# Performance work log

Measured on AMD Instinct MI355X. Metric: run time of the kernel, lower is better.

The kernel has to match this reference:

```python
import jax, jax.numpy as jnp
import numpy as np

HIDDEN = 4096
N_HEADS = 32
HEAD_DIM = HIDDEN // N_HEADS  # 128
ROPE_BASE = 10000.0


def _rotate_half(x):
    h = x.shape[-1] // 2
    return jnp.concatenate((-x[..., h:], x[..., :h]), axis=-1)


def _rope_sin_cos(position_ids):
    # position_ids: [B, S] int -> sin, cos: [B, 1, S, head_dim]
    inv_freq = 1.0 / (ROPE_BASE ** (jnp.arange(0, HEAD_DIM, 2, dtype=jnp.float32) / HEAD_DIM))
    freqs = position_ids.astype(jnp.float32)[..., None] * inv_freq  # [B,S,hd/2]
    emb = jnp.concatenate((freqs, freqs), axis=-1)  # [B,S,hd]
    return jnp.sin(emb)[:, None, :, :], jnp.cos(emb)[:, None, :, :]


def setup_inputs() -> dict:
    key = jax.random.key(0)
    k1, k2, k3 = jax.random.split(key, 3)
    B, S = 2, 2048
    hidden_states = jax.random.normal(k1, (B, S, HIDDEN), dtype=jnp.float32)
    w_qkv = jax.random.normal(k2, (HIDDEN, 3 * HIDDEN), dtype=jnp.float32) * 0.02
    wo = jax.random.normal(k3, (HIDDEN, HIDDEN), dtype=jnp.float32) * 0.02
    position_ids = jnp.broadcast_to(jnp.arange(S, dtype=jnp.int32)[None, :], (B, S))
    return {"hidden_states": hidden_states, "w_qkv": w_qkv, "wo": wo,
            "position_ids": position_ids}


def reference(hidden_states, w_qkv, wo, position_ids):
    B, S, H = hidden_states.shape
    qkv = hidden_states @ w_qkv  # [B,S,3H]
    q, k, v = jnp.split(qkv, 3, axis=-1)
    # [B,S,nH,hd] -> [B,nH,S,hd]
    q = q.reshape(B, S, N_HEADS, HEAD_DIM).transpose(0, 2, 1, 3)
    k = k.reshape(B, S, N_HEADS, HEAD_DIM).transpose(0, 2, 1, 3)
    v = v.reshape(B, S, N_HEADS, HEAD_DIM).transpose(0, 2, 1, 3)
    sin, cos = _rope_sin_cos(position_ids)  # [B,1,S,hd]
    q = q * cos + _rotate_half(q) * sin
    k = k * cos + _rotate_half(k) * sin
    scale = 1.0 / np.sqrt(HEAD_DIM)
    scores = jnp.einsum('bhqd,bhkd->bhqk', q, k) * scale
    causal = jnp.tril(jnp.ones((S, S), dtype=bool))
    scores = jnp.where(causal[None, None, :, :], scores, jnp.finfo(scores.dtype).min)
    attn = jax.nn.softmax(scores, axis=-1)
    out = jnp.einsum('bhqk,bhkd->bhqd', attn, v)  # [B,nH,S,hd]
    out = out.transpose(0, 2, 1, 3).reshape(B, S, H)
    return out @ wo
```

## Files before the change

### kernel.cpp

```cpp
#include <hip/hip_runtime.h>

typedef unsigned int u32;
typedef unsigned short u16;
typedef short short8 __attribute__((ext_vector_type(8)));
typedef float f32x4 __attribute__((ext_vector_type(4)));
typedef unsigned short us4 __attribute__((ext_vector_type(4)));

#define S_LEN 2048
#define BATCH 2
#define HID 4096
#define NH 32
#define HD 128
#define TRIH 12288

#define GCAST(p) ((const __attribute__((address_space(1))) u32*)(p))
#define LCAST(p) ((__attribute__((address_space(3))) u32*)(p))

static __device__ __forceinline__ u16 f2bf(float f) {
  union { float f; u32 u; } x; x.f = f;
  u32 u = x.u;
  u32 r = u + 0x7FFFu + ((u >> 16) & 1u);
  return (u16)(r >> 16);
}
static __device__ __forceinline__ float bf2f(u16 h) {
  union { u32 u; float f; } x; x.u = ((u32)h) << 16;
  return x.f;
}

__global__ __launch_bounds__(256) void cvt_f32_bf16(const float* __restrict__ in,
                                                    u16* __restrict__ out, int n4) {
  int i = blockIdx.x * 256 + threadIdx.x;
  if (i >= n4) return;
  float4 v = ((const float4*)in)[i];
  us4 o;
  o.x = f2bf(v.x); o.y = f2bf(v.y); o.z = f2bf(v.z); o.w = f2bf(v.w);
  ((us4*)out)[i] = o;
}

__global__ __launch_bounds__(256) void tr_cvt(const float* __restrict__ in,
                                              u16* __restrict__ out, int R, int C) {
  __shared__ float tile[32][33];
  int c0 = blockIdx.x * 32, r0 = blockIdx.y * 32;
  int tx = threadIdx.x, ty = threadIdx.y;
  for (int i = ty; i < 32; i += 8)
    tile[i][tx] = in[(size_t)(r0 + i) * C + c0 + tx];
  __syncthreads();
  for (int i = ty; i < 32; i += 8)
    out[(size_t)(c0 + i) * R + r0 + tx] = f2bf(tile[tx][i]);
}


template<int MQ, int NQ>
static __device__ __forceinline__ void mfma_quad(f32x4 (&acc)[8][4], short8 (&af)[4][2],
                                                 short8 (&bfr)[4][2]) {
#pragma unroll
  for (int ml = 0; ml < 4; ++ml)
#pragma unroll
    for (int nl = 0; nl < 2; ++nl) {
      acc[MQ*4+ml][NQ*2+nl] = __builtin_amdgcn_mfma_f32_16x16x32_bf16(
          af[ml][0], bfr[NQ*2+nl][0], acc[MQ*4+ml][NQ*2+nl], 0, 0, 0);
      acc[MQ*4+ml][NQ*2+nl] = __builtin_amdgcn_mfma_f32_16x16x32_bf16(
          af[ml][1], bfr[NQ*2+nl][1], acc[MQ*4+ml][NQ*2+nl], 0, 0, 0);
    }
}

template<int MQ>
static __device__ __forceinline__ void read_a(short8 (&af)[4][2], const u16* abase, int lane) {
#pragma unroll
  for (int ml = 0; ml < 4; ++ml) {
    int r = MQ*64 + ml*16 + (lane & 15);
#pragma unroll
    for (int kh = 0; kh < 2; ++kh) {
      int j = kh*4 + (lane >> 4);
      af[ml][kh] = *(const short8*)(abase + r*64 + ((j ^ (r & 7)) << 3));
    }
  }
}
template<int NQ>
static __device__ __forceinline__ void read_b(short8 (&bfr)[4][2], const u16* bbase,
                                              int rbase, int lane) {
#pragma unroll
  for (int nl = 0; nl < 2; ++nl) {
    int r = rbase + (NQ*2+nl)*16 + (lane & 15);
#pragma unroll
    for (int kh = 0; kh < 2; ++kh) {
      int j = kh*4 + (lane >> 4);
      bfr[NQ*2+nl][kh] = *(const short8*)(bbase + r*64 + ((j ^ (r & 7)) << 3));
    }
  }
}

#define PHASE_CLOSE() \
  __builtin_amdgcn_s_barrier(); \
  __builtin_amdgcn_sched_barrier(0);

#define SEAM_CLOSE(NSTR) \
  asm volatile("s_waitcnt vmcnt(" NSTR ")" ::: "memory"); \
  __builtin_amdgcn_s_barrier(); \
  __builtin_amdgcn_sched_barrier(0);

template<int OUTF32>
__global__ __launch_bounds__(512, 1) void gemm256(const u16* __restrict__ A,
                                                  const u16* __restrict__ Bt,
                                                  void* __restrict__ Cout,
                                                  int M, int N, int K, int nbm) {
  __shared__ __attribute__((aligned(16))) u16 lds[65536];
  const int tid = threadIdx.x, wave = tid >> 6, lane = tid & 63;
  const int wr = wave >> 2, wc = wave & 3;
  const int nwg = gridDim.x, wg = blockIdx.x, cpx = nwg >> 3;
  const int swz = (wg & 7) * cpx + (wg >> 3);
  const size_t tileM = (size_t)(swz % nbm) * 256;
  const size_t tileN = (size_t)(swz / nbm) * 256;
  const int nIter = K >> 7;

  const int r_ = tid >> 3;
  const int gc_ = (tid & 7) ^ (r_ & 7);

  const u16* Ag = A + tileM * K;
  const u16* Bg = Bt + tileN * K;

  f32x4 acc[8][4] = {};
  short8 af[4][2], bfr[4][2];

  auto stageA = [&](int kt, int buf, int half) {
    const u16* g0 = Ag + (size_t)(half*128 + r_) * K + kt*64 + (gc_ << 3);
    u16* l = lds + buf*16384 + half*8192 + wave*512;
    __builtin_amdgcn_global_load_lds(GCAST(g0), LCAST(l), 16, 0, 0);
    __builtin_amdgcn_global_load_lds(GCAST(g0 + (size_t)64*K), LCAST(l + 4096), 16, 0, 0);
  };
  auto stageB = [&](int kt, int buf, int half) {
    const u16* g0 = Bg + (size_t)(half*128 + r_) * K + kt*64 + (gc_ << 3);
    u16* l = lds + 32768 + buf*16384 + half*8192 + wave*512;
    __builtin_amdgcn_global_load_lds(GCAST(g0), LCAST(l), 16, 0, 0);
    __builtin_amdgcn_global_load_lds(GCAST(g0 + (size_t)64*K), LCAST(l + 4096), 16, 0, 0);
  };

  const u16* a0 = lds + wr*8192;
  const u16* a1 = lds + 16384 + wr*8192;
  const u16* b0 = lds + 32768 + (wc >> 1)*8192;
  const u16* b1 = lds + 32768 + 16384 + (wc >> 1)*8192;
  const int brb = (wc & 1) * 64;

  stageA(0, 0, 0); stageA(0, 0, 1);
  stageB(0, 0, 0); stageB(0, 0, 1);
  stageB(1, 1, 0); stageB(1, 1, 1);
  SEAM_CLOSE("4")

  for (int i = 0; i < nIter; ++i) {
    const int t1 = 2*i + 1, t2 = 2*i + 2, t3 = 2*i + 3;
    const bool more = (i + 1 < nIter);

    read_a<0>(af, a0, lane);
    read_b<0>(bfr, b0, brb, lane);
    read_b<1>(bfr, b0, brb, lane);
    stageA(t1, 1, 0); stageA(t1, 1, 1);
    __builtin_amdgcn_s_setprio(1);
    mfma_quad<0, 0>(acc, af, bfr);
    mfma_quad<0, 1>(acc, af, bfr);
    __builtin_amdgcn_s_setprio(0);
    PHASE_CLOSE()

    read_a<1>(af, a0, lane);
    if (more) { stageB(t2, 0, 0); stageB(t2, 0, 1); }
    __builtin_amdgcn_s_setprio(1);
    mfma_quad<1, 0>(acc, af, bfr);
    mfma_quad<1, 1>(acc, af, bfr);
    __builtin_amdgcn_s_setprio(0);
    if (more) { SEAM_CLOSE("4") } else { SEAM_CLOSE("0") }

    read_a<0>(af, a1, lane);
    read_b<0>(bfr, b1, brb, lane);
    read_b<1>(bfr, b1, brb, lane);
    if (more) { stageA(t2, 0, 0); stageA(t2, 0, 1); }
    __builtin_amdgcn_s_setprio(1);
    mfma_quad<0, 0>(acc, af, bfr);
    mfma_quad<0, 1>(acc, af, bfr);
    __builtin_amdgcn_s_setprio(0);
    PHASE_CLOSE()

    read_a<1>(af, a1, lane);
    if (more) { stageB(t3, 1, 0); stageB(t3, 1, 1); }
    __builtin_amdgcn_s_setprio(1);
    mfma_quad<1, 0>(acc, af, bfr);
    mfma_quad<1, 1>(acc, af, bfr);
    __builtin_amdgcn_s_setprio(0);
    if (more) { SEAM_CLOSE("4") } else { PHASE_CLOSE() }
  }

  const int r0o = (lane >> 4) << 2, c0o = lane & 15;
#pragma unroll
  for (int m = 0; m < 8; ++m)
#pragma unroll
    for (int n = 0; n < 4; ++n)
#pragma unroll
      for (int rr = 0; rr < 4; ++rr) {
        size_t grow = tileM + wr*128 + m*16 + r0o + rr;
        size_t gcol = tileN + wc*64 + n*16 + c0o;
        if (OUTF32) ((float*)Cout)[grow * N + gcol] = acc[m][n][rr];
        else        ((u16*)Cout)[grow * N + gcol] = f2bf(acc[m][n][rr]);
      }
}

__global__ __launch_bounds__(256) void rope_kernel(u16* __restrict__ qkv,
                                                   const int* __restrict__ pid) {
  int idx = blockIdx.x * 256 + threadIdx.x;
  int row = idx >> 12;
  int rem = idx & 4095;
  int which = rem >> 11;
  int rem2 = rem & 2047;
  int h = rem2 >> 6;
  int j = rem2 & 63;
  u16* p = qkv + (size_t)row * TRIH + which * HID + h * HD + j;
  float x0 = bf2f(p[0]), x1 = bf2f(p[64]);
  float pos = (float)pid[row];
  float invf = expf(-(float)j * 0.14391156831212787f);
  float th = pos * invf;
  float sn, cs;
  sincosf(th, &sn, &cs);
  p[0]  = f2bf(x0 * cs - x1 * sn);
  p[64] = f2bf(x1 * cs + x0 * sn);
}

__global__ __launch_bounds__(512, 2) void attn_kernel(const u16* __restrict__ qkv,
                                                      u16* __restrict__ O) {
  const int bid = blockIdx.x;
  const int qt = 15 - (bid >> 6);
  const int bh = bid & 63;
  const int b = bh >> 5, h = bh & 31;
  const int tid = threadIdx.x, wave = tid >> 6, lane = tid & 63;
  __shared__ u16 Ks[64 * 128];
  __shared__ u16 VsT[128 * 64];
  __shared__ u16 Ps[8][16 * 64];
  const u16* base = qkv + (size_t)b * S_LEN * TRIH + h * HD;

  const int rbase = (lane >> 4) << 2;
  const int cbase = lane & 15;
  const int q_lo = qt * 128;
  const int wrow0 = q_lo + wave * 16;

  short8 qf[4];
  {
    const u16* qrow = base + (size_t)(wrow0 + cbase) * TRIH;
#pragma unroll
    for (int f = 0; f < 4; ++f)
      qf[f] = *(const short8*)(qrow + ((f * 4 + (lane >> 4)) << 3));
  }

  const int tmax_w = 2 * qt + (wave >= 4 ? 1 : 0);
  const int tmax_b = 2 * qt + 1;

  float mrun[4], lrun[4];
  f32x4 accO[8] = {};
#pragma unroll
  for (int r = 0; r < 4; ++r) { mrun[r] = -1e30f; lrun[r] = 0.f; }

  short8 kreg[2], vreg[2];
#pragma unroll
  for (int it = 0; it < 2; ++it) {
    int c = tid + it * 512;
    int row = c >> 4, ch = c & 15;
    const u16* src = base + (size_t)row * TRIH + (ch << 3);
    kreg[it] = *(const short8*)(src + HID);
    vreg[it] = *(const short8*)(src + 2 * HID);
  }

  for (int t = 0; t <= tmax_b; ++t) {
    __syncthreads();
#pragma unroll
    for (int it = 0; it < 2; ++it) {
      int c = tid + it * 512;
      int row = c >> 4, ch = c & 15;
      *(short8*)(Ks + row * 128 + ((ch ^ (row & 7)) << 3)) = kreg[it];
#pragma unroll
      for (int i = 0; i < 8; ++i) {
        int d = (ch << 3) + i;
        VsT[d * 64 + (((row >> 3) ^ (ch & 7)) << 3) + (row & 7)] = (u16)vreg[it][i];
      }
    }
    __syncthreads();

    if (t < tmax_b) {
      int kv1 = (t + 1) << 6;
#pragma unroll
      for (int it = 0; it < 2; ++it) {
        int c = tid + it * 512;
        int row = c >> 4, ch = c & 15;
        const u16* src = base + (size_t)(kv1 + row) * TRIH + (ch << 3);
        kreg[it] = *(const short8*)(src + HID);
        vreg[it] = *(const short8*)(src + 2 * HID);
      }
    }

    if (t > tmax_w) continue;

    f32x4 s[4] = {};
#pragma unroll
    for (int n = 0; n < 4; ++n) {
      int krow = n * 16 + cbase;
#pragma unroll
      for (int f = 0; f < 4; ++f) {
        int ch = f * 4 + (lane >> 4);
        short8 kf = *(const short8*)(Ks + krow * 128 + ((ch ^ (krow & 7)) << 3));
        s[n] = __builtin_amdgcn_mfma_f32_16x16x32_bf16(qf[f], kf, s[n], 0, 0, 0);
      }
    }
    const float scale = 0.08838834764831845f;
    const int kv0 = t << 6;
    if (t == tmax_w) {
#pragma unroll
      for (int n = 0; n < 4; ++n)
#pragma unroll
        for (int r = 0; r < 4; ++r) {
          int kvcol = kv0 + n * 16 + cbase;
          int qrow = wrow0 + rbase + r;
          s[n][r] = (kvcol <= qrow) ? s[n][r] * scale : -1e30f;
        }
    } else {
#pragma unroll
      for (int n = 0; n < 4; ++n) s[n] *= scale;
    }

    float tmax[4];
#pragma unroll
    for (int r = 0; r < 4; ++r) {
      float tm = fmaxf(fmaxf(s[0][r], s[1][r]), fmaxf(s[2][r], s[3][r]));
      tm = fmaxf(tm, __shfl_xor(tm, 1));
      tm = fmaxf(tm, __shfl_xor(tm, 2));
      tm = fmaxf(tm, __shfl_xor(tm, 4));
      tm = fmaxf(tm, __shfl_xor(tm, 8));
      tmax[r] = tm;
    }
    bool need = false;
#pragma unroll
    for (int r = 0; r < 4; ++r) need |= (tmax[r] > mrun[r] + 8.0f);
    if (__any(need)) {
#pragma unroll
      for (int r = 0; r < 4; ++r) {
        float mnew = fmaxf(mrun[r], tmax[r]);
        float corr = __expf(mrun[r] - mnew);
        float rs = 0.f;
#pragma unroll
        for (int n = 0; n < 4; ++n) { float pv = __expf(s[n][r] - mnew); s[n][r] = pv; rs += pv; }
        rs += __shfl_xor(rs, 1); rs += __shfl_xor(rs, 2);
        rs += __shfl_xor(rs, 4); rs += __shfl_xor(rs, 8);
        lrun[r] = lrun[r] * corr + rs;
        mrun[r] = mnew;
#pragma unroll
        for (int nd = 0; nd < 8; ++nd) accO[nd][r] *= corr;
      }
    } else {
#pragma unroll
      for (int r = 0; r < 4; ++r) {
        float rs = 0.f;
#pragma unroll
        for (int n = 0; n < 4; ++n) { float pv = __expf(s[n][r] - mrun[r]); s[n][r] = pv; rs += pv; }
        rs += __shfl_xor(rs, 1); rs += __shfl_xor(rs, 2);
        rs += __shfl_xor(rs, 4); rs += __shfl_xor(rs, 8);
        lrun[r] += rs;
      }
    }

    u16* Pw = (u16*)Ps[wave];
#pragma unroll
    for (int n = 0; n < 4; ++n)
#pragma unroll
      for (int r = 0; r < 4; ++r) {
        int rl = rbase + r;
        int col = n * 16 + cbase;
        Pw[rl * 64 + (((col >> 3) ^ (rl & 7)) << 3) + (col & 7)] = f2bf(s[n][r]);
      }

    short8 pa[2];
    {
      int prow = lane & 15;
#pragma unroll
      for (int f2 = 0; f2 < 2; ++f2) {
        int ch = f2 * 4 + (lane >> 4);
        pa[f2] = *(const short8*)(Pw + prow * 64 + ((ch ^ (prow & 7)) << 3));
      }
    }
#pragma unroll
    for (int nd = 0; nd < 8; ++nd) {
      int drow = nd * 16 + cbase;
#pragma unroll
      for (int f2 = 0; f2 < 2; ++f2) {
        int ch = f2 * 4 + (lane >> 4);
        short8 vb = *(const short8*)(VsT + drow * 64 + ((ch ^ ((drow >> 3) & 7)) << 3));
        accO[nd] = __builtin_amdgcn_mfma_f32_16x16x32_bf16(pa[f2], vb, accO[nd], 0, 0, 0);
      }
    }
  }

#pragma unroll
  for (int nd = 0; nd < 8; ++nd)
#pragma unroll
    for (int r = 0; r < 4; ++r) {
      int qrow = wrow0 + rbase + r;
      int col = h * HD + nd * 16 + cbase;
      O[(size_t)(b * S_LEN + qrow) * HID + col] = f2bf(accO[nd][r] / lrun[r]);
    }
}

extern "C" void kernel_launch(void* const* d_in, const int* in_sizes, int n_in,
                              void* d_out, int out_size, void* d_ws, size_t ws_size,
                              hipStream_t stream) {
  const float* hidden = (const float*)d_in[0];
  const float* w_qkv  = (const float*)d_in[1];
  const float* wo     = (const float*)d_in[2];
  const int*   pid    = (const int*)d_in[3];

  const size_t MB = 1024ull * 1024ull;
  u16* hb    = (u16*)d_ws;
  u16* wqkvT = (u16*)((char*)d_ws + 32 * MB);
  u16* woT   = (u16*)((char*)d_ws + 128 * MB);
  u16* qkvb  = (u16*)((char*)d_ws + 160 * MB);
  u16* Obuf  = hb;

  cvt_f32_bf16<<<16384, 256, 0, stream>>>(hidden, hb, (BATCH * S_LEN * HID) / 4);
  dim3 tb(32, 8);
  tr_cvt<<<dim3(TRIH / 32, HID / 32), tb, 0, stream>>>(w_qkv, wqkvT, HID, TRIH);
  tr_cvt<<<dim3(HID / 32, HID / 32), tb, 0, stream>>>(wo, woT, HID, HID);

  gemm256<0><<<768, 512, 0, stream>>>(hb, wqkvT, qkvb, BATCH * S_LEN, TRIH, HID, 16);

  rope_kernel<<<(BATCH * S_LEN * 2 * NH * 64) / 256, 256, 0, stream>>>(qkvb, pid);

  attn_kernel<<<1024, 512, 0, stream>>>(qkvb, Obuf);

  gemm256<1><<<256, 512, 0, stream>>>(Obuf, woT, d_out, BATCH * S_LEN, HID, HID, 16);
}
```

Measured before the change: 822.0 us.

## Double-buffer K/V tiles in attention and vectorize RoPE kernel

The attention kernel now keeps two shared-memory K/V buffers and writes the next tile into the alternate buffer while the current one is computed. This drops one __syncthreads per iteration and lets global loads run two tiles ahead. Shared memory per block grows from about 48KB to about 80KB, which may limit blocks per CU. Separately, the RoPE kernel now has each thread handle 8 contiguous elements with 16-byte vector loads and stores instead of scalar u16 accesses, with the grid shrunk to match.

```diff
diff --git a/kernel.cpp b/kernel.cpp
--- a/kernel.cpp
+++ b/kernel.cpp
@@ -204,21 +204,27 @@
 __global__ __launch_bounds__(256) void rope_kernel(u16* __restrict__ qkv,
                                                    const int* __restrict__ pid) {
   int idx = blockIdx.x * 256 + threadIdx.x;
-  int row = idx >> 12;
-  int rem = idx & 4095;
-  int which = rem >> 11;
-  int rem2 = rem & 2047;
-  int h = rem2 >> 6;
-  int j = rem2 & 63;
-  u16* p = qkv + (size_t)row * TRIH + which * HID + h * HD + j;
-  float x0 = bf2f(p[0]), x1 = bf2f(p[64]);
+  int row = idx >> 9;
+  int rem = idx & 511;
+  int which = rem >> 8;
+  int h = (rem >> 3) & 31;
+  int j0 = (rem & 7) << 3;
+  u16* p = qkv + (size_t)row * TRIH + which * HID + h * HD + j0;
+  short8 lo = *(short8*)p;
+  short8 hi = *(short8*)(p + 64);
   float pos = (float)pid[row];
-  float invf = expf(-(float)j * 0.14391156831212787f);
-  float th = pos * invf;
-  float sn, cs;
-  sincosf(th, &sn, &cs);
-  p[0]  = f2bf(x0 * cs - x1 * sn);
-  p[64] = f2bf(x1 * cs + x0 * sn);
+  short8 olo, ohi;
+#pragma unroll
+  for (int i = 0; i < 8; ++i) {
+    float x0 = bf2f((u16)lo[i]), x1 = bf2f((u16)hi[i]);
+    float th = pos * expf(-(float)(j0 + i) * 0.14391156831212787f);
+    float sn, cs;
+    sincosf(th, &sn, &cs);
+    olo[i] = (short)f2bf(x0 * cs - x1 * sn);
+    ohi[i] = (short)f2bf(x1 * cs + x0 * sn);
+  }
+  *(short8*)p = olo;
+  *(short8*)(p + 64) = ohi;
 }
 
 __global__ __launch_bounds__(512, 2) void attn_kernel(const u16* __restrict__ qkv,
@@ -228,8 +234,8 @@
   const int bh = bid & 63;
   const int b = bh >> 5, h = bh & 31;
   const int tid = threadIdx.x, wave = tid >> 6, lane = tid & 63;
-  __shared__ u16 Ks[64 * 128];
-  __shared__ u16 VsT[128 * 64];
+  __shared__ u16 Ks[2][64 * 128];
+  __shared__ u16 VsT[2][128 * 64];
   __shared__ u16 Ps[8][16 * 64];
   const u16* base = qkv + (size_t)b * S_LEN * TRIH + h * HD;
 
@@ -255,41 +261,40 @@
   for (int r = 0; r < 4; ++r) { mrun[r] = -1e30f; lrun[r] = 0.f; }
 
   short8 kreg[2], vreg[2];
-#pragma unroll
-  for (int it = 0; it < 2; ++it) {
-    int c = tid + it * 512;
-    int row = c >> 4, ch = c & 15;
-    const u16* src = base + (size_t)row * TRIH + (ch << 3);
-    kreg[it] = *(const short8*)(src + HID);
-    vreg[it] = *(const short8*)(src + 2 * HID);
-  }
-
-  for (int t = 0; t <= tmax_b; ++t) {
-    __syncthreads();
+  auto load_tile = [&](int t) {
+    int kv = t << 6;
 #pragma unroll
     for (int it = 0; it < 2; ++it) {
       int c = tid + it * 512;
       int row = c >> 4, ch = c & 15;
-      *(short8*)(Ks + row * 128 + ((ch ^ (row & 7)) << 3)) = kreg[it];
+      const u16* src = base + (size_t)(kv + row) * TRIH + (ch << 3);
+      kreg[it] = *(const short8*)(src + HID);
+      vreg[it] = *(const short8*)(src + 2 * HID);
+    }
+  };
+  auto write_tile = [&](int buf) {
+#pragma unroll
+    for (int it = 0; it < 2; ++it) {
+      int c = tid + it * 512;
+      int row = c >> 4, ch = c & 15;
+      *(short8*)(Ks[buf] + row * 128 + ((ch ^ (row & 7)) << 3)) = kreg[it];
 #pragma unroll
       for (int i = 0; i < 8; ++i) {
         int d = (ch << 3) + i;
-        VsT[d * 64 + (((row >> 3) ^ (ch & 7)) << 3) + (row & 7)] = (u16)vreg[it][i];
-      }
-    }
+        VsT[buf][d * 64 + (((row >> 3) ^ (ch & 7)) << 3) + (row & 7)] = (u16)vreg[it][i];
+      }
+    }
+  };
+
+  load_tile(0);
+  write_tile(0);
+  load_tile(1);
+
+  for (int t = 0; t <= tmax_b; ++t) {
+    const int cur = t & 1;
     __syncthreads();
-
-    if (t < tmax_b) {
-      int kv1 = (t + 1) << 6;
-#pragma unroll
-      for (int it = 0; it < 2; ++it) {
-        int c = tid + it * 512;
-        int row = c >> 4, ch = c & 15;
-        const u16* src = base + (size_t)(kv1 + row) * TRIH + (ch << 3);
-        kreg[it] = *(const short8*)(src + HID);
-        vreg[it] = *(const short8*)(src + 2 * HID);
-      }
-    }
+    if (t < tmax_b) write_tile(cur ^ 1);
+    if (t + 2 <= tmax_b) load_tile(t + 2);
 
     if (t > tmax_w) continue;
 
@@ -300,7 +305,7 @@
 #pragma unroll
       for (int f = 0; f < 4; ++f) {
         int ch = f * 4 + (lane >> 4);
-        short8 kf = *(const short8*)(Ks + krow * 128 + ((ch ^ (krow & 7)) << 3));
+        short8 kf = *(const short8*)(Ks[cur] + krow * 128 + ((ch ^ (krow & 7)) << 3));
         s[n] = __builtin_amdgcn_mfma_f32_16x16x32_bf16(qf[f], kf, s[n], 0, 0, 0);
       }
     }
@@ -385,7 +390,7 @@
 #pragma unroll
       for (int f2 = 0; f2 < 2; ++f2) {
         int ch = f2 * 4 + (lane >> 4);
-        short8 vb = *(const short8*)(VsT + drow * 64 + ((ch ^ ((drow >> 3) & 7)) << 3));
+        short8 vb = *(const short8*)(VsT[cur] + drow * 64 + ((ch ^ ((drow >> 3) & 7)) << 3));
         accO[nd] = __builtin_amdgcn_mfma_f32_16x16x32_bf16(pa[f2], vb, accO[nd], 0, 0, 0);
       }
     }
@@ -423,7 +428,7 @@
 
   gemm256<0><<<768, 512, 0, stream>>>(hb, wqkvT, qkvb, BATCH * S_LEN, TRIH, HID, 16);
 
-  rope_kernel<<<(BATCH * S_LEN * 2 * NH * 64) / 256, 256, 0, stream>>>(qkvb, pid);
+  rope_kernel<<<(BATCH * S_LEN * 2 * NH * 8) / 256, 256, 0, stream>>>(qkvb, pid);
 
   attn_kernel<<<1024, 512, 0, stream>>>(qkvb, Obuf);
 
```

Result: no change. 815.6 us (-0.8%).
